# Performance work log

Measured on AMD Instinct MI355X. Metric: run time of the kernel, lower is better.

Reference implementation:

```python
import jax, jax.numpy as jnp
import numpy as np

D_MODEL, DFF, OUT, SEQ = 256, 1024, 32, 512
SIGMA = 0.1          # sigma for q/k/v/z SMC noise
SIGMA_OBS = 0.5      # observation noise


def _layernorm(x, g, b, eps=1e-6):
    mu = jnp.mean(x, axis=-1, keepdims=True)
    var = jnp.mean(jnp.square(x - mu), axis=-1, keepdims=True)
    return (x - mu) * jax.lax.rsqrt(var + eps) * g + b


def _resample(params, i_t, t):
    # params: (B,P,S,D); i_t: (B,P) ancestor indices; resample only the past [:t+1]
    past = jnp.take_along_axis(params[:, :, :t + 1, :], i_t[:, :, None, None], axis=1)
    return jnp.concatenate([past, params[:, :, t + 1:, :]], axis=2)


def setup_inputs() -> dict:
    key = jax.random.key(0)
    ks = jax.random.split(key, 24)
    B, P = 32, 10
    d = {
        'x': jax.random.normal(ks[0], (B, P, D_MODEL), jnp.float32),
        'y': jax.random.normal(ks[1], (B, P, OUT), jnp.float32),
        'K': jax.random.normal(ks[2], (B, P, SEQ, D_MODEL), jnp.float32),
        'V': jax.random.normal(ks[3], (B, P, SEQ, D_MODEL), jnp.float32),
        'R': jax.random.normal(ks[4], (B, P, SEQ, D_MODEL), jnp.float32),
        'noise_q': jax.random.normal(ks[5], (B, P, 1, D_MODEL), jnp.float32),
        'noise_k': jax.random.normal(ks[6], (B, P, 1, D_MODEL), jnp.float32),
        'noise_v': jax.random.normal(ks[7], (B, P, 1, D_MODEL), jnp.float32),
        'noise_z': jax.random.normal(ks[8], (B, P, 1, D_MODEL), jnp.float32),
        'dec_timestep': 256,
    }
    s = 0.02
    d['wq_w'] = jax.random.normal(ks[9], (D_MODEL, D_MODEL), jnp.float32) * s
    d['wq_b'] = jnp.zeros((D_MODEL,), jnp.float32)
    d['wk_w'] = jax.random.normal(ks[10], (D_MODEL, D_MODEL), jnp.float32) * s
    d['wk_b'] = jnp.zeros((D_MODEL,), jnp.float32)
    d['wv_w'] = jax.random.normal(ks[11], (D_MODEL, D_MODEL), jnp.float32) * s
    d['wv_b'] = jnp.zeros((D_MODEL,), jnp.float32)
    d['wz_w'] = jax.random.normal(ks[12], (D_MODEL, D_MODEL), jnp.float32) * s
    d['wz_b'] = jnp.zeros((D_MODEL,), jnp.float32)
    d['ln1_g'] = jnp.ones((D_MODEL,), jnp.float32)
    d['ln1_b'] = jnp.zeros((D_MODEL,), jnp.float32)
    d['ffn_w1'] = jax.random.normal(ks[13], (D_MODEL, DFF), jnp.float32) * s
    d['ffn_b1'] = jnp.zeros((DFF,), jnp.float32)
    d['ffn_w2'] = jax.random.normal(ks[14], (DFF, D_MODEL), jnp.float32) * s
    d['ffn_b2'] = jnp.zeros((D_MODEL,), jnp.float32)
    d['ln2_g'] = jnp.ones((D_MODEL,), jnp.float32)
    d['ln2_b'] = jnp.zeros((D_MODEL,), jnp.float32)
    d['out_w'] = jax.random.normal(ks[15], (D_MODEL, OUT), jnp.float32) * s
    d['out_b'] = jnp.zeros((OUT,), jnp.float32)
    return d


def reference(x, y, K, V, R, noise_q, noise_k, noise_v, noise_z,
              wq_w, wq_b, wk_w, wk_b, wv_w, wv_b, wz_w, wz_b,
              ln1_g, ln1_b, ffn_w1, ffn_b1, ffn_w2, ffn_b2,
              ln2_g, ln2_b, out_w, out_b, dec_timestep):
    t = dec_timestep
    B, P, D = x.shape
    sq = jnp.sqrt(jnp.float32(SIGMA))
    xq = x[:, :, None, :]           # (B,P,1,D)
    yq = y[:, :, None, :]           # (B,P,1,F_y)
    # --- Self_Attention_SMC: project current token, add SMC gaussian noise ---
    q = xq @ wq_w + wq_b + sq * noise_q
    k = xq @ wk_w + wk_b + sq * noise_k
    v = xq @ wv_w + wv_b + sq * noise_v
    # in-place style KV cache update at timestep t (concat past/new/future)
    K = jnp.concatenate([K[:, :, :t, :], k, K[:, :, t + 1:, :]], axis=2)
    V = jnp.concatenate([V[:, :, :t, :], v, V[:, :, t + 1:, :]], axis=2)
    logits = jnp.einsum('bpod,bpsd->bpos', q, K) / jnp.sqrt(jnp.float32(D))
    attn_weights = jax.nn.softmax(logits, axis=-1)          # (B,P,1,S)
    z = jnp.einsum('bpos,bpsd->bpod', attn_weights, V)
    z = z @ wz_w + wz_b + sq * noise_z
    # --- full_model: layernorm + FFN + layernorm ---
    out = _layernorm(z + xq, ln1_g, ln1_b)
    r = jax.nn.relu(out @ ffn_w1 + ffn_b1) @ ffn_w2 + ffn_b2
    r = _layernorm(r + out, ln2_g, ln2_b)                   # (B,P,1,D)
    predictions = r @ out_w + out_b                          # (B,P,1,F_y)
    R = jnp.concatenate([R[:, :, :t, :], r, R[:, :, t + 1:, :]], axis=2)
    mu = jnp.squeeze(yq - predictions, axis=-2)              # (B,P,F_y)
    log_w = -jnp.sum(mu * mu, axis=-1) / (2.0 * SIGMA_OBS)   # (B,P)
    w = jax.nn.softmax(jnp.exp(log_w), axis=-1)              # faithful to original (softmax of exp)
    w = jax.lax.stop_gradient(w)
    # categorical resampling of ancestors (tf.random.categorical uses w as logits)
    i_t = jax.random.categorical(jax.random.key(42), w[:, None, :], shape=(B, P))
    i_t = jax.lax.stop_gradient(i_t)
    K = _resample(K, i_t, t)
    V = _resample(V, i_t, t)
    R = _resample(R, i_t, t)
    return r, attn_weights, K, V, R, w
```

## Files before the change

### kernel.cpp

```cpp
#include <hip/hip_runtime.h>
#include <hip/hip_bf16.h>
#include <stdint.h>

#define BATCH 32
#define NPART 10
#define BP_TOT 320
#define DM 256
#define FF 1024
#define OD 32
#define SL 512

#define SQRT_SIGMA 0.31622776601683794f

__device__ __forceinline__ uint32_t rotl32(uint32_t x, uint32_t r) {
    return (x << r) | (x >> (32u - r));
}

__device__ __forceinline__ void threefry2x32(uint32_t k0, uint32_t k1,
                                             uint32_t x0, uint32_t x1,
                                             uint32_t& o0, uint32_t& o1) {
    uint32_t k2 = k0 ^ k1 ^ 0x1BD11BDAu;
    uint32_t x = x0 + k0, y = x1 + k1;
#define TFR(r) { x += y; y = rotl32(y, r); y ^= x; }
    TFR(13u) TFR(15u) TFR(26u) TFR(6u)
    x += k1; y += k2 + 1u;
    TFR(17u) TFR(29u) TFR(16u) TFR(24u)
    x += k2; y += k0 + 2u;
    TFR(13u) TFR(15u) TFR(26u) TFR(6u)
    x += k0; y += k1 + 3u;
    TFR(17u) TFR(29u) TFR(16u) TFR(24u)
    x += k1; y += k2 + 4u;
    TFR(13u) TFR(15u) TFR(26u) TFR(6u)
    x += k2; y += k0 + 5u;
#undef TFR
    o0 = x; o1 = y;
}

__device__ __forceinline__ float jax_gumbel_part(uint32_t m) {
    const float TINY = 1.17549435e-38f;
    uint32_t o0, o1;
    threefry2x32(0u, 42u, 0u, m, o0, o1);
    uint32_t bits = o0 ^ o1;
    uint32_t fb = (bits >> 9) | 0x3f800000u;
    float f = __uint_as_float(fb) - 1.0f;
    float u = fmaxf(TINY, f + TINY);
    return -logf(-logf(u));
}

__global__ __launch_bounds__(256) void qkv_kernel(
    const float* __restrict__ x,
    const float* __restrict__ nq, const float* __restrict__ nk,
    const float* __restrict__ nv,
    const float* __restrict__ wq_w, const float* __restrict__ wq_b,
    const float* __restrict__ wk_w, const float* __restrict__ wk_b,
    const float* __restrict__ wv_w, const float* __restrict__ wv_b,
    float* __restrict__ qtmp, float* __restrict__ knew, float* __restrict__ vnew)
{
    const int bp = blockIdx.x;
    const int m  = blockIdx.y;
    const int d  = threadIdx.x;

    __shared__ float xs[DM];
    xs[d] = x[bp * DM + d];
    __syncthreads();

    const float* W; const float* bias; const float* noise; float* outp;
    if (m == 0)      { W = wq_w; bias = wq_b; noise = nq; outp = qtmp + (size_t)bp * SL; }
    else if (m == 1) { W = wk_w; bias = wk_b; noise = nk; outp = knew + (size_t)bp * DM; }
    else             { W = wv_w; bias = wv_b; noise = nv; outp = vnew + (size_t)bp * DM; }

    float a0 = 0.f, a1 = 0.f, a2 = 0.f, a3 = 0.f;
    #pragma unroll 4
    for (int i = 0; i < 64; ++i) {
        a0 = fmaf(xs[i],       W[(i      ) * DM + d], a0);
        a1 = fmaf(xs[i +  64], W[(i +  64) * DM + d], a1);
        a2 = fmaf(xs[i + 128], W[(i + 128) * DM + d], a2);
        a3 = fmaf(xs[i + 192], W[(i + 192) * DM + d], a3);
    }
    outp[d] = (a0 + a1) + (a2 + a3) + bias[d] + SQRT_SIGMA * noise[bp * DM + d];
}

__global__ __launch_bounds__(1024) void attn_kernel(
    const float* __restrict__ Kin, const float* __restrict__ Vin,
    const float* __restrict__ knew, const float* __restrict__ vnew,
    const int* __restrict__ t_ptr,
    float* __restrict__ attn_out, float* __restrict__ ztmp)
{
    const int bp   = blockIdx.x;
    const int tid  = threadIdx.x;
    const int lane = tid & 63;
    const int wave = tid >> 6;
    const int t    = *t_ptr;

    __shared__ float qs[DM], ks[DM], vs[DM];
    __shared__ float att[SL];
    __shared__ float scratch[16 * 256];
    __shared__ float red[32];

    if (tid < DM) {
        qs[tid] = attn_out[(size_t)bp * SL + tid];
        ks[tid] = knew[(size_t)bp * DM + tid];
        vs[tid] = vnew[(size_t)bp * DM + tid];
    }
    __syncthreads();

    const float* Kbp = Kin + (size_t)bp * SL * DM;
    const float* Vbp = Vin + (size_t)bp * SL * DM;
    float4 q4 = *(const float4*)&qs[lane * 4];
    const int s0 = wave * 32;

    for (int j0 = 0; j0 < 32; j0 += 8) {
        float4 k4[8];
        #pragma unroll
        for (int u = 0; u < 8; ++u) {
            int s = s0 + j0 + u;
            k4[u] = (s == t) ? *(const float4*)&ks[lane * 4]
                             : *(const float4*)&Kbp[(size_t)s * DM + lane * 4];
        }
        #pragma unroll
        for (int u = 0; u < 8; ++u) {
            float acc = q4.x * k4[u].x + q4.y * k4[u].y + q4.z * k4[u].z + q4.w * k4[u].w;
            #pragma unroll
            for (int off = 32; off; off >>= 1) acc += __shfl_down(acc, off);
            if (lane == 0) att[s0 + j0 + u] = acc * 0.0625f;
        }
    }
    __syncthreads();

    {
        float l = (tid < SL) ? att[tid] : -3.402823466e+38f;
        float m = l;
        #pragma unroll
        for (int off = 32; off; off >>= 1) m = fmaxf(m, __shfl_down(m, off));
        if (lane == 0) red[wave] = m;
        __syncthreads();
        float gm = red[0];
        #pragma unroll
        for (int i = 1; i < 16; ++i) gm = fmaxf(gm, red[i]);
        float e = (tid < SL) ? expf(l - gm) : 0.f;
        float ssum = e;
        #pragma unroll
        for (int off = 32; off; off >>= 1) ssum += __shfl_down(ssum, off);
        if (lane == 0) red[16 + wave] = ssum;
        __syncthreads();
        float tot = 0.f;
        #pragma unroll
        for (int i = 0; i < 16; ++i) tot += red[16 + i];
        float a = e / tot;
        if (tid < SL) {
            att[tid] = a;
            attn_out[(size_t)bp * SL + tid] = a;
        }
    }
    __syncthreads();

    {
        float4 z4 = make_float4(0.f, 0.f, 0.f, 0.f);
        for (int j0 = 0; j0 < 32; j0 += 8) {
            float4 v4[8];
            #pragma unroll
            for (int u = 0; u < 8; ++u) {
                int s = s0 + j0 + u;
                v4[u] = (s == t) ? *(const float4*)&vs[lane * 4]
                                 : *(const float4*)&Vbp[(size_t)s * DM + lane * 4];
            }
            #pragma unroll
            for (int u = 0; u < 8; ++u) {
                float a = att[s0 + j0 + u];
                z4.x = fmaf(a, v4[u].x, z4.x);
                z4.y = fmaf(a, v4[u].y, z4.y);
                z4.z = fmaf(a, v4[u].z, z4.z);
                z4.w = fmaf(a, v4[u].w, z4.w);
            }
        }
        *(float4*)&scratch[wave * 256 + lane * 4] = z4;
    }
    __syncthreads();
    if (tid < DM) {
        float z = 0.f;
        #pragma unroll
        for (int w = 0; w < 16; ++w) z += scratch[w * 256 + tid];
        ztmp[(size_t)bp * DM + tid] = z;
    }
}

__global__ __launch_bounds__(1024) void post_kernel(
    const float* __restrict__ x, const float* __restrict__ nz,
    const float* __restrict__ wz_w, const float* __restrict__ wz_b,
    const float* __restrict__ ln1_g, const float* __restrict__ ln1_b,
    const float* __restrict__ w1, const float* __restrict__ b1,
    const float* __restrict__ w2, const float* __restrict__ b2,
    const float* __restrict__ ln2_g, const float* __restrict__ ln2_b,
    float* __restrict__ r_out)
{
    const int bp   = blockIdx.x;
    const int tid  = threadIdx.x;
    const int lane = tid & 63;
    const int wave = tid >> 6;
    const int grp  = tid >> 8;
    const int qtid = tid & 255;

    __shared__ float buf[DM];
    __shared__ float xs[DM];
    __shared__ float hid[FF];
    __shared__ float scratch[1024];
    __shared__ float red[32];

    if (tid < DM) {
        buf[tid] = r_out[(size_t)bp * DM + tid];
        xs[tid]  = x[bp * DM + tid];
    }
    __syncthreads();

    {
        const int i0 = grp * 64;
        float a0 = 0.f, a1 = 0.f;
        #pragma unroll 4
        for (int ii = 0; ii < 32; ++ii) {
            a0 = fmaf(buf[i0 + ii],      wz_w[(i0 + ii)      * DM + qtid], a0);
            a1 = fmaf(buf[i0 + ii + 32], wz_w[(i0 + ii + 32) * DM + qtid], a1);
        }
        scratch[grp * 256 + qtid] = a0 + a1;
    }
    __syncthreads();
    float h = 0.f;
    if (tid < DM) {
        float az = (scratch[tid] + scratch[256 + tid]) + (scratch[512 + tid] + scratch[768 + tid]);
        h = az + wz_b[tid] + SQRT_SIGMA * nz[bp * DM + tid] + xs[tid];
    }

    float s1 = h;
    #pragma unroll
    for (int off = 32; off; off >>= 1) s1 += __shfl_down(s1, off);
    if (lane == 0) red[wave] = s1;
    __syncthreads();
    float mu = (red[0] + red[1] + red[2] + red[3]) * (1.0f / DM);
    float dv = (tid < DM) ? (h - mu) : 0.f;
    float s2 = dv * dv;
    #pragma unroll
    for (int off = 32; off; off >>= 1) s2 += __shfl_down(s2, off);
    if (lane == 0) red[16 + wave] = s2;
    __syncthreads();
    float var = (red[16] + red[17] + red[18] + red[19]) * (1.0f / DM);
    float o = 0.f;
    __syncthreads();
    if (tid < DM) {
        o = dv * rsqrtf(var + 1e-6f) * ln1_g[tid] + ln1_b[tid];
        buf[tid] = o;
    }
    __syncthreads();

    {
        float h0 = 0.f, h1 = 0.f, h2 = 0.f, h3 = 0.f;
        #pragma unroll 4
        for (int i = 0; i < 64; ++i) {
            h0 = fmaf(buf[i],       w1[(i      ) * FF + tid], h0);
            h1 = fmaf(buf[i +  64], w1[(i +  64) * FF + tid], h1);
            h2 = fmaf(buf[i + 128], w1[(i + 128) * FF + tid], h2);
            h3 = fmaf(buf[i + 192], w1[(i + 192) * FF + tid], h3);
        }
        hid[tid] = fmaxf((h0 + h1) + (h2 + h3) + b1[tid], 0.f);
    }
    __syncthreads();

    {
        const int i0 = grp * 256;
        float a0 = 0.f, a1 = 0.f, a2 = 0.f, a3 = 0.f;
        #pragma unroll 4
        for (int ii = 0; ii < 64; ++ii) {
            a0 = fmaf(hid[i0 + ii],       w2[(i0 + ii      ) * DM + qtid], a0);
            a1 = fmaf(hid[i0 + ii +  64], w2[(i0 + ii +  64) * DM + qtid], a1);
            a2 = fmaf(hid[i0 + ii + 128], w2[(i0 + ii + 128) * DM + qtid], a2);
            a3 = fmaf(hid[i0 + ii + 192], w2[(i0 + ii + 192) * DM + qtid], a3);
        }
        scratch[grp * 256 + qtid] = (a0 + a1) + (a2 + a3);
    }
    __syncthreads();
    float rr = 0.f;
    if (tid < DM) {
        rr = (scratch[tid] + scratch[256 + tid]) + (scratch[512 + tid] + scratch[768 + tid])
           + b2[tid] + o;
    }

    float t1 = rr;
    #pragma unroll
    for (int off = 32; off; off >>= 1) t1 += __shfl_down(t1, off);
    if (lane == 0) red[wave] = t1;
    __syncthreads();
    float mu2 = (red[0] + red[1] + red[2] + red[3]) * (1.0f / DM);
    float dv2 = (tid < DM) ? (rr - mu2) : 0.f;
    float t2 = dv2 * dv2;
    #pragma unroll
    for (int off = 32; off; off >>= 1) t2 += __shfl_down(t2, off);
    if (lane == 0) red[16 + wave] = t2;
    __syncthreads();
    float var2 = (red[16] + red[17] + red[18] + red[19]) * (1.0f / DM);
    if (tid < DM) {
        float rf = dv2 * rsqrtf(var2 + 1e-6f) * ln2_g[tid] + ln2_b[tid];
        r_out[(size_t)bp * DM + tid] = rf;
    }
}

__global__ __launch_bounds__(320) void weights_kernel(
    const float* __restrict__ r, const float* __restrict__ y,
    const float* __restrict__ out_w, const float* __restrict__ out_b,
    float* __restrict__ w_out, int* __restrict__ i_t)
{
    const int b   = blockIdx.x;
    const int tid = threadIdx.x;
    const int p   = tid >> 5;
    const int j   = tid & 31;

    __shared__ float sred[NPART];
    __shared__ float es[NPART];
    __shared__ float pe[NPART];
    __shared__ float wsm[NPART];

    const float* rrow = r + (size_t)(b * NPART + p) * DM;
    float acc = 0.f;
    #pragma unroll 4
    for (int i = 0; i < DM; ++i) acc = fmaf(rrow[i], out_w[i * OD + j], acc);
    float pred = acc + out_b[j];
    float muv  = y[(size_t)(b * NPART + p) * OD + j] - pred;
    float s    = muv * muv;
    #pragma unroll
    for (int off = 16; off; off >>= 1) s += __shfl_down(s, off, 32);
    if (j == 0) sred[p] = s;
    __syncthreads();

    if (tid < NPART) es[tid] = expf(-sred[tid]);
    __syncthreads();
    if (tid < NPART) {
        float mx = es[0];
        #pragma unroll
        for (int i = 1; i < NPART; ++i) mx = fmaxf(mx, es[i]);
        pe[tid] = expf(es[tid] - mx);
    }
    __syncthreads();
    if (tid < NPART) {
        float sum = 0.f;
        #pragma unroll
        for (int i = 0; i < NPART; ++i) sum += pe[i];
        float wv = pe[tid] / sum;
        w_out[b * NPART + tid] = wv;
        wsm[tid] = wv;
    }
    __syncthreads();

    if (tid < NPART) {
        int pp = tid;
        int best = 0;
        float bests = -3.402823466e+38f;
        #pragma unroll
        for (int jj = 0; jj < NPART; ++jj) {
            uint32_t m = (uint32_t)(b * 100 + pp * 10 + jj);
            float score = jax_gumbel_part(m) + wsm[jj];
            if (score > bests) { bests = score; best = jj; }
        }
        i_t[b * NPART + pp] = best;
    }
}

__global__ __launch_bounds__(256) void resample_kernel(
    const float* __restrict__ Kin, const float* __restrict__ Vin,
    const float* __restrict__ Rin,
    const float* __restrict__ knew, const float* __restrict__ vnew,
    const float* __restrict__ rnew,
    const int* __restrict__ i_t, const int* __restrict__ t_ptr,
    float* __restrict__ Kout, float* __restrict__ Vout, float* __restrict__ Rout)
{
    const int t      = *t_ptr;
    const int tensor = blockIdx.y;
    const int tid    = threadIdx.x;
    size_t idx  = (size_t)blockIdx.x * 256 + tid;
    int lane4 = (int)(idx & 63);
    int row   = (int)(idx >> 6);
    int bpi   = row >> 9;
    int s     = row & 511;
    int b     = bpi / NPART;
    int p     = bpi - b * NPART;
    int srcp  = (s <= t) ? i_t[bpi] : p;
    int src_bpi = b * NPART + srcp;

    const float* src;
    if (s == t) {
        const float* nb = (tensor == 0) ? knew : (tensor == 1) ? vnew : rnew;
        src = nb + (size_t)src_bpi * DM;
    } else {
        const float* base = (tensor == 0) ? Kin : (tensor == 1) ? Vin : Rin;
        src = base + ((size_t)src_bpi * SL + s) * DM;
    }
    float* outb = (tensor == 0) ? Kout : (tensor == 1) ? Vout : Rout;
    float4 v4 = *(const float4*)(src + (size_t)lane4 * 4);
    *(float4*)(outb + (size_t)row * DM + (size_t)lane4 * 4) = v4;
}

extern "C" void kernel_launch(void* const* d_in, const int* in_sizes, int n_in,
                              void* d_out, int out_size, void* d_ws, size_t ws_size,
                              hipStream_t stream) {
    const float* x    = (const float*)d_in[0];
    const float* y    = (const float*)d_in[1];
    const float* Kin  = (const float*)d_in[2];
    const float* Vin  = (const float*)d_in[3];
    const float* Rin  = (const float*)d_in[4];
    const float* nq   = (const float*)d_in[5];
    const float* nk   = (const float*)d_in[6];
    const float* nv   = (const float*)d_in[7];
    const float* nz   = (const float*)d_in[8];
    const int*   tptr = (const int*)d_in[9];
    const float* wq_w = (const float*)d_in[10];
    const float* wq_b = (const float*)d_in[11];
    const float* wk_w = (const float*)d_in[12];
    const float* wk_b = (const float*)d_in[13];
    const float* wv_w = (const float*)d_in[14];
    const float* wv_b = (const float*)d_in[15];
    const float* wz_w = (const float*)d_in[16];
    const float* wz_b = (const float*)d_in[17];
    const float* ln1g = (const float*)d_in[18];
    const float* ln1b = (const float*)d_in[19];
    const float* w1   = (const float*)d_in[20];
    const float* b1   = (const float*)d_in[21];
    const float* w2   = (const float*)d_in[22];
    const float* b2   = (const float*)d_in[23];
    const float* ln2g = (const float*)d_in[24];
    const float* ln2b = (const float*)d_in[25];
    const float* outw = (const float*)d_in[26];
    const float* outb = (const float*)d_in[27];

    float* out = (float*)d_out;
    const size_t R_ELEMS    = (size_t)BP_TOT * DM;
    const size_t ATTN_ELEMS = (size_t)BP_TOT * SL;
    const size_t KVR_ELEMS  = (size_t)BP_TOT * SL * DM;
    float* r_out    = out;
    float* attn_out = out + R_ELEMS;
    float* K_out    = out + R_ELEMS + ATTN_ELEMS;
    float* V_out    = K_out + KVR_ELEMS;
    float* R_out    = V_out + KVR_ELEMS;
    float* w_out    = R_out + KVR_ELEMS;

    float* knew = (float*)d_ws;
    float* vnew = knew + R_ELEMS;
    int*   i_t  = (int*)(vnew + R_ELEMS);

    qkv_kernel<<<dim3(BP_TOT, 3), 256, 0, stream>>>(
        x, nq, nk, nv, wq_w, wq_b, wk_w, wk_b, wv_w, wv_b,
        attn_out, knew, vnew);

    attn_kernel<<<BP_TOT, 1024, 0, stream>>>(
        Kin, Vin, knew, vnew, tptr, attn_out, r_out);

    post_kernel<<<BP_TOT, 1024, 0, stream>>>(
        x, nz, wz_w, wz_b, ln1g, ln1b, w1, b1, w2, b2, ln2g, ln2b,
        r_out);

    weights_kernel<<<BATCH, 320, 0, stream>>>(
        r_out, y, outw, outb, w_out, i_t);

    resample_kernel<<<dim3(163840 / 4, 3), 256, 0, stream>>>(
        Kin, Vin, Rin, knew, vnew, r_out, i_t, tptr,
        K_out, V_out, R_out);
}
```

Baseline: 355.8 us.

## Split attention into logits and softmax-AV kernels across sequence chunks

Replaces the single 1024-thread attention kernel per particle with two kernels, each launched over 4 sequence chunks of 256 threads. The first writes raw logits to scratch. The second recomputes the softmax redundantly in each chunk, accumulates a partial attention-times-V sum, and writes it to a partials buffer that the post kernel adds up. The aim is more blocks and better occupancy when streaming K and V. The cost is an extra launch, a round trip of logits through global memory, and reusing the K_out and V_out output buffers as scratch before the resample kernel overwrites them.

```diff
diff --git a/kernel.cpp b/kernel.cpp
--- a/kernel.cpp
+++ b/kernel.cpp
@@ -80,34 +80,28 @@
     outp[d] = (a0 + a1) + (a2 + a3) + bias[d] + SQRT_SIGMA * noise[bp * DM + d];
 }
 
-__global__ __launch_bounds__(1024) void attn_kernel(
-    const float* __restrict__ Kin, const float* __restrict__ Vin,
-    const float* __restrict__ knew, const float* __restrict__ vnew,
-    const int* __restrict__ t_ptr,
-    float* __restrict__ attn_out, float* __restrict__ ztmp)
+__global__ __launch_bounds__(256) void logits_kernel(
+    const float* __restrict__ Kin, const float* __restrict__ knew,
+    const float* __restrict__ qtmp, const int* __restrict__ t_ptr,
+    float* __restrict__ logits)
 {
     const int bp   = blockIdx.x;
+    const int sc   = blockIdx.y;
     const int tid  = threadIdx.x;
     const int lane = tid & 63;
     const int wave = tid >> 6;
     const int t    = *t_ptr;
 
-    __shared__ float qs[DM], ks[DM], vs[DM];
-    __shared__ float att[SL];
-    __shared__ float scratch[16 * 256];
-    __shared__ float red[32];
-
-    if (tid < DM) {
-        qs[tid] = attn_out[(size_t)bp * SL + tid];
+    __shared__ float qs[DM], ks[DM];
+    if (tid < DM) {
+        qs[tid] = qtmp[(size_t)bp * SL + tid];
         ks[tid] = knew[(size_t)bp * DM + tid];
-        vs[tid] = vnew[(size_t)bp * DM + tid];
     }
     __syncthreads();
 
     const float* Kbp = Kin + (size_t)bp * SL * DM;
-    const float* Vbp = Vin + (size_t)bp * SL * DM;
     float4 q4 = *(const float4*)&qs[lane * 4];
-    const int s0 = wave * 32;
+    const int s0 = sc * 128 + wave * 32;
 
     for (int j0 = 0; j0 < 32; j0 += 8) {
         float4 k4[8];
@@ -122,70 +116,84 @@
             float acc = q4.x * k4[u].x + q4.y * k4[u].y + q4.z * k4[u].z + q4.w * k4[u].w;
             #pragma unroll
             for (int off = 32; off; off >>= 1) acc += __shfl_down(acc, off);
-            if (lane == 0) att[s0 + j0 + u] = acc * 0.0625f;
-        }
-    }
-    __syncthreads();
-
-    {
-        float l = (tid < SL) ? att[tid] : -3.402823466e+38f;
-        float m = l;
-        #pragma unroll
-        for (int off = 32; off; off >>= 1) m = fmaxf(m, __shfl_down(m, off));
-        if (lane == 0) red[wave] = m;
-        __syncthreads();
-        float gm = red[0];
-        #pragma unroll
-        for (int i = 1; i < 16; ++i) gm = fmaxf(gm, red[i]);
-        float e = (tid < SL) ? expf(l - gm) : 0.f;
-        float ssum = e;
-        #pragma unroll
-        for (int off = 32; off; off >>= 1) ssum += __shfl_down(ssum, off);
-        if (lane == 0) red[16 + wave] = ssum;
-        __syncthreads();
-        float tot = 0.f;
-        #pragma unroll
-        for (int i = 0; i < 16; ++i) tot += red[16 + i];
-        float a = e / tot;
-        if (tid < SL) {
-            att[tid] = a;
-            attn_out[(size_t)bp * SL + tid] = a;
-        }
-    }
-    __syncthreads();
-
-    {
-        float4 z4 = make_float4(0.f, 0.f, 0.f, 0.f);
-        for (int j0 = 0; j0 < 32; j0 += 8) {
-            float4 v4[8];
-            #pragma unroll
-            for (int u = 0; u < 8; ++u) {
-                int s = s0 + j0 + u;
-                v4[u] = (s == t) ? *(const float4*)&vs[lane * 4]
-                                 : *(const float4*)&Vbp[(size_t)s * DM + lane * 4];
-            }
-            #pragma unroll
-            for (int u = 0; u < 8; ++u) {
-                float a = att[s0 + j0 + u];
-                z4.x = fmaf(a, v4[u].x, z4.x);
-                z4.y = fmaf(a, v4[u].y, z4.y);
-                z4.z = fmaf(a, v4[u].z, z4.z);
-                z4.w = fmaf(a, v4[u].w, z4.w);
-            }
-        }
-        *(float4*)&scratch[wave * 256 + lane * 4] = z4;
-    }
-    __syncthreads();
-    if (tid < DM) {
-        float z = 0.f;
-        #pragma unroll
-        for (int w = 0; w < 16; ++w) z += scratch[w * 256 + tid];
-        ztmp[(size_t)bp * DM + tid] = z;
+            if (lane == 0) logits[(size_t)bp * SL + s0 + j0 + u] = acc * 0.0625f;
+        }
+    }
+}
+
+__global__ __launch_bounds__(256) void attnz_kernel(
+    const float* __restrict__ Vin, const float* __restrict__ vnew,
+    const float* __restrict__ logits, const int* __restrict__ t_ptr,
+    float* __restrict__ attn_out, float* __restrict__ zpart)
+{
+    const int bp   = blockIdx.x;
+    const int sc   = blockIdx.y;
+    const int tid  = threadIdx.x;
+    const int lane = tid & 63;
+    const int wave = tid >> 6;
+    const int t    = *t_ptr;
+
+    __shared__ float att[SL];
+    __shared__ float vs[DM];
+    __shared__ float scratch[4 * 256];
+    __shared__ float red[8];
+
+    if (tid < DM) vs[tid] = vnew[(size_t)bp * DM + tid];
+
+    float l0 = logits[(size_t)bp * SL + tid];
+    float l1 = logits[(size_t)bp * SL + tid + 256];
+    float m = fmaxf(l0, l1);
+    #pragma unroll
+    for (int off = 32; off; off >>= 1) m = fmaxf(m, __shfl_down(m, off));
+    if (lane == 0) red[wave] = m;
+    __syncthreads();
+    float gm = fmaxf(fmaxf(red[0], red[1]), fmaxf(red[2], red[3]));
+    float e0 = expf(l0 - gm), e1 = expf(l1 - gm);
+    float ssum = e0 + e1;
+    #pragma unroll
+    for (int off = 32; off; off >>= 1) ssum += __shfl_down(ssum, off);
+    if (lane == 0) red[4 + wave] = ssum;
+    __syncthreads();
+    float inv = 1.0f / (red[4] + red[5] + red[6] + red[7]);
+    float a0 = e0 * inv, a1 = e1 * inv;
+    att[tid] = a0; att[tid + 256] = a1;
+    if (sc == 0) {
+        attn_out[(size_t)bp * SL + tid]       = a0;
+        attn_out[(size_t)bp * SL + tid + 256] = a1;
+    }
+    __syncthreads();
+
+    const float* Vbp = Vin + (size_t)bp * SL * DM;
+    const int s0 = sc * 128 + wave * 32;
+    float4 z4 = make_float4(0.f, 0.f, 0.f, 0.f);
+    for (int j0 = 0; j0 < 32; j0 += 8) {
+        float4 v4[8];
+        #pragma unroll
+        for (int u = 0; u < 8; ++u) {
+            int s = s0 + j0 + u;
+            v4[u] = (s == t) ? *(const float4*)&vs[lane * 4]
+                             : *(const float4*)&Vbp[(size_t)s * DM + lane * 4];
+        }
+        #pragma unroll
+        for (int u = 0; u < 8; ++u) {
+            float a = att[s0 + j0 + u];
+            z4.x = fmaf(a, v4[u].x, z4.x);
+            z4.y = fmaf(a, v4[u].y, z4.y);
+            z4.z = fmaf(a, v4[u].z, z4.z);
+            z4.w = fmaf(a, v4[u].w, z4.w);
+        }
+    }
+    *(float4*)&scratch[wave * 256 + lane * 4] = z4;
+    __syncthreads();
+    if (tid < DM) {
+        float zp = (scratch[tid] + scratch[256 + tid]) + (scratch[512 + tid] + scratch[768 + tid]);
+        zpart[(size_t)bp * 1024 + sc * 256 + tid] = zp;
     }
 }
 
 __global__ __launch_bounds__(1024) void post_kernel(
     const float* __restrict__ x, const float* __restrict__ nz,
+    const float* __restrict__ zpart,
     const float* __restrict__ wz_w, const float* __restrict__ wz_b,
     const float* __restrict__ ln1_g, const float* __restrict__ ln1_b,
     const float* __restrict__ w1, const float* __restrict__ b1,
@@ -207,7 +215,8 @@
     __shared__ float red[32];
 
     if (tid < DM) {
-        buf[tid] = r_out[(size_t)bp * DM + tid];
+        const float* zp = zpart + (size_t)bp * 1024;
+        buf[tid] = (zp[tid] + zp[256 + tid]) + (zp[512 + tid] + zp[768 + tid]);
         xs[tid]  = x[bp * DM + tid];
     }
     __syncthreads();
@@ -442,15 +451,21 @@
     float* vnew = knew + R_ELEMS;
     int*   i_t  = (int*)(vnew + R_ELEMS);
 
+    float* logits = K_out;
+    float* zpart  = V_out;
+
     qkv_kernel<<<dim3(BP_TOT, 3), 256, 0, stream>>>(
         x, nq, nk, nv, wq_w, wq_b, wk_w, wk_b, wv_w, wv_b,
         attn_out, knew, vnew);
 
-    attn_kernel<<<BP_TOT, 1024, 0, stream>>>(
-        Kin, Vin, knew, vnew, tptr, attn_out, r_out);
+    logits_kernel<<<dim3(BP_TOT, 4), 256, 0, stream>>>(
+        Kin, knew, attn_out, tptr, logits);
+
+    attnz_kernel<<<dim3(BP_TOT, 4), 256, 0, stream>>>(
+        Vin, vnew, logits, tptr, attn_out, zpart);
 
     post_kernel<<<BP_TOT, 1024, 0, stream>>>(
-        x, nz, wz_w, wz_b, ln1g, ln1b, w1, b1, w2, b2, ln2g, ln2b,
+        x, nz, zpart, wz_w, wz_b, ln1g, ln1b, w1, b1, w2, b2, ln2g, ln2b,
         r_out);
 
     weights_kernel<<<BATCH, 320, 0, stream>>>(
```

Result: faster. 342.3 us (-3.8%).

## Split attention over sequence chunks and fuse future-row K/V copy into attention

Applied to the files above, without the earlier changes.

Attention is split into four sequence chunks per particle, each computing local softmax statistics and partial z, followed by a combine kernel that rescales them flash-style. While K and V are already loaded for attention, rows after t are written directly to the K/V outputs, so the resample kernel skips those rows for K and V. This aims to avoid re-reading most of K and V from memory and to raise parallelism with smaller blocks. In exchange it adds an extra kernel launch and uses the R output buffer as scratch, which R resampling later overwrites.

```diff
diff --git a/kernel.cpp b/kernel.cpp
--- a/kernel.cpp
+++ b/kernel.cpp
@@ -80,25 +80,28 @@
     outp[d] = (a0 + a1) + (a2 + a3) + bias[d] + SQRT_SIGMA * noise[bp * DM + d];
 }
 
-__global__ __launch_bounds__(1024) void attn_kernel(
+__global__ __launch_bounds__(256) void attn_chunk_kernel(
     const float* __restrict__ Kin, const float* __restrict__ Vin,
     const float* __restrict__ knew, const float* __restrict__ vnew,
-    const int* __restrict__ t_ptr,
-    float* __restrict__ attn_out, float* __restrict__ ztmp)
+    const float* __restrict__ qtmp, const int* __restrict__ t_ptr,
+    float* __restrict__ Kout, float* __restrict__ Vout,
+    float* __restrict__ logits, float* __restrict__ zpart,
+    float* __restrict__ mstat)
 {
     const int bp   = blockIdx.x;
+    const int sc   = blockIdx.y;
     const int tid  = threadIdx.x;
     const int lane = tid & 63;
     const int wave = tid >> 6;
     const int t    = *t_ptr;
 
     __shared__ float qs[DM], ks[DM], vs[DM];
-    __shared__ float att[SL];
-    __shared__ float scratch[16 * 256];
-    __shared__ float red[32];
-
-    if (tid < DM) {
-        qs[tid] = attn_out[(size_t)bp * SL + tid];
+    __shared__ float att_loc[128];
+    __shared__ float scratch[4 * 256];
+    __shared__ float redm[2], rede[2];
+
+    if (tid < DM) {
+        qs[tid] = qtmp[(size_t)bp * SL + tid];
         ks[tid] = knew[(size_t)bp * DM + tid];
         vs[tid] = vnew[(size_t)bp * DM + tid];
     }
@@ -107,7 +110,7 @@
     const float* Kbp = Kin + (size_t)bp * SL * DM;
     const float* Vbp = Vin + (size_t)bp * SL * DM;
     float4 q4 = *(const float4*)&qs[lane * 4];
-    const int s0 = wave * 32;
+    const int s0 = sc * 128 + wave * 32;
 
     for (int j0 = 0; j0 < 32; j0 += 8) {
         float4 k4[8];
@@ -119,69 +122,93 @@
         }
         #pragma unroll
         for (int u = 0; u < 8; ++u) {
+            int s = s0 + j0 + u;
+            if (s > t) *(float4*)(Kout + ((size_t)bp * SL + s) * DM + lane * 4) = k4[u];
             float acc = q4.x * k4[u].x + q4.y * k4[u].y + q4.z * k4[u].z + q4.w * k4[u].w;
             #pragma unroll
             for (int off = 32; off; off >>= 1) acc += __shfl_down(acc, off);
-            if (lane == 0) att[s0 + j0 + u] = acc * 0.0625f;
-        }
-    }
-    __syncthreads();
-
-    {
-        float l = (tid < SL) ? att[tid] : -3.402823466e+38f;
-        float m = l;
-        #pragma unroll
-        for (int off = 32; off; off >>= 1) m = fmaxf(m, __shfl_down(m, off));
-        if (lane == 0) red[wave] = m;
-        __syncthreads();
-        float gm = red[0];
-        #pragma unroll
-        for (int i = 1; i < 16; ++i) gm = fmaxf(gm, red[i]);
-        float e = (tid < SL) ? expf(l - gm) : 0.f;
-        float ssum = e;
-        #pragma unroll
-        for (int off = 32; off; off >>= 1) ssum += __shfl_down(ssum, off);
-        if (lane == 0) red[16 + wave] = ssum;
-        __syncthreads();
-        float tot = 0.f;
-        #pragma unroll
-        for (int i = 0; i < 16; ++i) tot += red[16 + i];
-        float a = e / tot;
-        if (tid < SL) {
-            att[tid] = a;
-            attn_out[(size_t)bp * SL + tid] = a;
-        }
-    }
-    __syncthreads();
-
-    {
-        float4 z4 = make_float4(0.f, 0.f, 0.f, 0.f);
-        for (int j0 = 0; j0 < 32; j0 += 8) {
-            float4 v4[8];
-            #pragma unroll
-            for (int u = 0; u < 8; ++u) {
-                int s = s0 + j0 + u;
-                v4[u] = (s == t) ? *(const float4*)&vs[lane * 4]
-                                 : *(const float4*)&Vbp[(size_t)s * DM + lane * 4];
+            if (lane == 0) {
+                float l = acc * 0.0625f;
+                att_loc[wave * 32 + j0 + u] = l;
+                logits[(size_t)bp * SL + s] = l;
             }
-            #pragma unroll
-            for (int u = 0; u < 8; ++u) {
-                float a = att[s0 + j0 + u];
-                z4.x = fmaf(a, v4[u].x, z4.x);
-                z4.y = fmaf(a, v4[u].y, z4.y);
-                z4.z = fmaf(a, v4[u].z, z4.z);
-                z4.w = fmaf(a, v4[u].w, z4.w);
-            }
-        }
-        *(float4*)&scratch[wave * 256 + lane * 4] = z4;
-    }
-    __syncthreads();
-    if (tid < DM) {
-        float z = 0.f;
-        #pragma unroll
-        for (int w = 0; w < 16; ++w) z += scratch[w * 256 + tid];
-        ztmp[(size_t)bp * DM + tid] = z;
-    }
+        }
+    }
+    __syncthreads();
+
+    float l = (tid < 128) ? att_loc[tid] : -3.402823466e+38f;
+    float mm = l;
+    #pragma unroll
+    for (int off = 32; off; off >>= 1) mm = fmaxf(mm, __shfl_down(mm, off));
+    if (tid < 128 && lane == 0) redm[wave] = mm;
+    __syncthreads();
+    const float m_loc = fmaxf(redm[0], redm[1]);
+    float p = (tid < 128) ? expf(l - m_loc) : 0.f;
+    if (tid < 128) att_loc[tid] = p;
+    float e = p;
+    #pragma unroll
+    for (int off = 32; off; off >>= 1) e += __shfl_down(e, off);
+    if (tid < 128 && lane == 0) rede[wave] = e;
+    __syncthreads();
+    const float e_loc = rede[0] + rede[1];
+
+    float4 z4 = make_float4(0.f, 0.f, 0.f, 0.f);
+    for (int j0 = 0; j0 < 32; j0 += 8) {
+        float4 v4[8];
+        #pragma unroll
+        for (int u = 0; u < 8; ++u) {
+            int s = s0 + j0 + u;
+            v4[u] = (s == t) ? *(const float4*)&vs[lane * 4]
+                             : *(const float4*)&Vbp[(size_t)s * DM + lane * 4];
+        }
+        #pragma unroll
+        for (int u = 0; u < 8; ++u) {
+            int s = s0 + j0 + u;
+            if (s > t) *(float4*)(Vout + ((size_t)bp * SL + s) * DM + lane * 4) = v4[u];
+            float a = att_loc[wave * 32 + j0 + u];
+            z4.x = fmaf(a, v4[u].x, z4.x);
+            z4.y = fmaf(a, v4[u].y, z4.y);
+            z4.z = fmaf(a, v4[u].z, z4.z);
+            z4.w = fmaf(a, v4[u].w, z4.w);
+        }
+    }
+    *(float4*)&scratch[wave * 256 + lane * 4] = z4;
+    __syncthreads();
+    if (tid < DM) {
+        float zp = (scratch[tid] + scratch[256 + tid]) + (scratch[512 + tid] + scratch[768 + tid]);
+        zpart[((size_t)bp * 4 + sc) * DM + tid] = zp;
+    }
+    if (tid == 0) {
+        mstat[((size_t)bp * 4 + sc) * 2 + 0] = m_loc;
+        mstat[((size_t)bp * 4 + sc) * 2 + 1] = e_loc;
+    }
+}
+
+__global__ __launch_bounds__(256) void attn_combine_kernel(
+    const float* __restrict__ logits, const float* __restrict__ zpart,
+    const float* __restrict__ mstat,
+    float* __restrict__ attn_out, float* __restrict__ ztmp)
+{
+    const int bp  = blockIdx.x;
+    const int tid = threadIdx.x;
+
+    const float* ms = mstat + (size_t)bp * 8;
+    float m0 = ms[0], e0 = ms[1], m1 = ms[2], e1 = ms[3];
+    float m2 = ms[4], e2 = ms[5], m3 = ms[6], e3 = ms[7];
+    float gm = fmaxf(fmaxf(m0, m1), fmaxf(m2, m3));
+    float f0 = expf(m0 - gm), f1 = expf(m1 - gm);
+    float f2 = expf(m2 - gm), f3 = expf(m3 - gm);
+    float inv = 1.0f / (e0 * f0 + e1 * f1 + e2 * f2 + e3 * f3);
+
+    float l0 = logits[(size_t)bp * SL + tid];
+    float l1 = logits[(size_t)bp * SL + tid + 256];
+    attn_out[(size_t)bp * SL + tid]       = expf(l0 - gm) * inv;
+    attn_out[(size_t)bp * SL + tid + 256] = expf(l1 - gm) * inv;
+
+    const float* zp = zpart + (size_t)bp * 4 * DM;
+    float z = (zp[tid] * f0 + zp[DM + tid] * f1)
+            + (zp[2 * DM + tid] * f2 + zp[3 * DM + tid] * f3);
+    ztmp[(size_t)bp * DM + tid] = z * inv;
 }
 
 __global__ __launch_bounds__(1024) void post_kernel(
@@ -369,14 +396,17 @@
     const int* __restrict__ i_t, const int* __restrict__ t_ptr,
     float* __restrict__ Kout, float* __restrict__ Vout, float* __restrict__ Rout)
 {
-    const int t      = *t_ptr;
-    const int tensor = blockIdx.y;
-    const int tid    = threadIdx.x;
+    const int t    = *t_ptr;
+    const int ysel = blockIdx.y;
+    const int tid  = threadIdx.x;
     size_t idx  = (size_t)blockIdx.x * 256 + tid;
     int lane4 = (int)(idx & 63);
     int row   = (int)(idx >> 6);
     int bpi   = row >> 9;
     int s     = row & 511;
+
+    if (ysel != 2 && s > t) return;
+
     int b     = bpi / NPART;
     int p     = bpi - b * NPART;
     int srcp  = (s <= t) ? i_t[bpi] : p;
@@ -384,13 +414,13 @@
 
     const float* src;
     if (s == t) {
-        const float* nb = (tensor == 0) ? knew : (tensor == 1) ? vnew : rnew;
+        const float* nb = (ysel == 1) ? knew : (ysel == 0) ? vnew : rnew;
         src = nb + (size_t)src_bpi * DM;
     } else {
-        const float* base = (tensor == 0) ? Kin : (tensor == 1) ? Vin : Rin;
+        const float* base = (ysel == 1) ? Kin : (ysel == 0) ? Vin : Rin;
         src = base + ((size_t)src_bpi * SL + s) * DM;
     }
-    float* outb = (tensor == 0) ? Kout : (tensor == 1) ? Vout : Rout;
+    float* outb = (ysel == 1) ? Kout : (ysel == 0) ? Vout : Rout;
     float4 v4 = *(const float4*)(src + (size_t)lane4 * 4);
     *(float4*)(outb + (size_t)row * DM + (size_t)lane4 * 4) = v4;
 }
@@ -442,12 +472,20 @@
     float* vnew = knew + R_ELEMS;
     int*   i_t  = (int*)(vnew + R_ELEMS);
 
+    float* logits = R_out;
+    float* zpart  = R_out + ATTN_ELEMS;
+    float* mstat  = zpart + (size_t)BP_TOT * 4 * DM;
+
     qkv_kernel<<<dim3(BP_TOT, 3), 256, 0, stream>>>(
         x, nq, nk, nv, wq_w, wq_b, wk_w, wk_b, wv_w, wv_b,
         attn_out, knew, vnew);
 
-    attn_kernel<<<BP_TOT, 1024, 0, stream>>>(
-        Kin, Vin, knew, vnew, tptr, attn_out, r_out);
+    attn_chunk_kernel<<<dim3(BP_TOT, 4), 256, 0, stream>>>(
+        Kin, Vin, knew, vnew, attn_out, tptr,
+        K_out, V_out, logits, zpart, mstat);
+
+    attn_combine_kernel<<<BP_TOT, 256, 0, stream>>>(
+        logits, zpart, mstat, attn_out, r_out);
 
     post_kernel<<<BP_TOT, 1024, 0, stream>>>(
         x, nz, wz_w, wz_b, ln1g, ln1b, w1, b1, w2, b2, ln2g, ln2b,
```

After: 337.8 us. -5.1%, faster.
